# Optimization experiments

Measured on AMD Instinct MI355X. Metric: run time of the kernel, lower is better.

## Reference

```python
import jax, jax.numpy as jnp
import numpy as np

B, N, M, D, NHEAD, FF, C, K = 2, 16384, 2048, 256, 8, 512, 50, 3
HID = 128          # embed/pos hidden
HEAD_HID = 256     # seg head hidden
L = 4              # depth
EPS = 1e-5


def setup_inputs() -> dict:
    key = jax.random.key(0)
    ks = jax.random.split(key, 32)
    g = lambda i, shape: jax.random.normal(ks[i], shape, dtype=jnp.float32) * 0.02
    z = lambda shape: jnp.zeros(shape, jnp.float32)
    o = lambda shape: jnp.ones(shape, jnp.float32)
    return {
        "xyz": jax.random.normal(ks[0], (B, N, 3), dtype=jnp.float32),
        "embed_w1": g(1, (3, HID)), "embed_b1": z((HID,)),
        "embed_w2": g(2, (HID, D)), "embed_b2": z((D,)),
        "pos_w1": g(3, (3, HID)), "pos_b1": z((HID,)),
        "pos_w2": g(4, (HID, D)), "pos_b2": z((D,)),
        "Wq": g(5, (L, D, D)), "bq": z((L, D)),
        "Wk": g(6, (L, D, D)), "bk": z((L, D)),
        "Wv": g(7, (L, D, D)), "bv": z((L, D)),
        "Wo": g(8, (L, D, D)), "bo": z((L, D)),
        "ln1_s": o((L, D)), "ln1_b": z((L, D)),
        "W1": g(9, (L, D, FF)), "b1": z((L, FF)),
        "W2": g(10, (L, FF, D)), "b2": z((L, D)),
        "ln2_s": o((L, D)), "ln2_b": z((L, D)),
        "head_w1": g(11, (D, HEAD_HID)), "head_b1": z((HEAD_HID,)),
        "head_w2": g(12, (HEAD_HID, C)), "head_b2": z((C,)),
    }


def _ln(x, s, b):
    m = x.mean(-1, keepdims=True)
    v = ((x - m) ** 2).mean(-1, keepdims=True)
    return (x - m) / jnp.sqrt(v + EPS) * s + b


def reference(xyz, embed_w1, embed_b1, embed_w2, embed_b2,
              pos_w1, pos_b1, pos_w2, pos_b2,
              Wq, bq, Wk, bk, Wv, bv, Wo, bo, ln1_s, ln1_b,
              W1, b1, W2, b2, ln2_s, ln2_b,
              head_w1, head_b1, head_w2, head_b2):
    # deterministic token subsample (replaces randperm stub): strided pick of M points
    stride = N // M
    tok = xyz[:, ::stride, :][:, :M]                                  # [B,M,3]
    # per-point embed + learned positional encoding
    x = jax.nn.relu(tok @ embed_w1 + embed_b1) @ embed_w2 + embed_b2  # [B,M,D]
    x = x + jax.nn.relu(tok @ pos_w1 + pos_b1) @ pos_w2 + pos_b2
    dh = D // NHEAD
    scale = 1.0 / jnp.sqrt(jnp.float32(dh))

    def layer(x, p):
        wq, bq_, wk, bk_, wv, bv_, wo, bo_, l1s, l1b, w1, b1_, w2, b2_, l2s, l2b = p
        # pre-norm MHSA
        y = _ln(x, l1s, l1b)
        q = (y @ wq + bq_).reshape(B, M, NHEAD, dh)
        k = (y @ wk + bk_).reshape(B, M, NHEAD, dh)
        v = (y @ wv + bv_).reshape(B, M, NHEAD, dh)
        att = jax.nn.softmax(jnp.einsum('bqhd,bkhd->bhqk', q, k) * scale, axis=-1)
        o = jnp.einsum('bhqk,bkhd->bqhd', att, v).reshape(B, M, D)
        x = x + o @ wo + bo_
        # pre-norm FFN (gelu, exact erf as in torch)
        y = _ln(x, l2s, l2b)
        x = x + jax.nn.gelu(y @ w1 + b1_, approximate=False) @ w2 + b2_
        return x, None

    x, _ = jax.lax.scan(layer, x, (Wq, bq, Wk, bk, Wv, bv, Wo, bo,
                                   ln1_s, ln1_b, W1, b1, W2, b2, ln2_s, ln2_b))
    logits_tok = jax.nn.relu(x @ head_w1 + head_b1) @ head_w2 + head_b2  # [B,M,C]

    # kNN propagation N->M: dist^2 = |q|^2 + |k|^2 - 2 q.k, topk smallest
    q2 = (xyz ** 2).sum(-1)[..., None]            # [B,N,1]
    k2 = (tok ** 2).sum(-1)[:, None, :]           # [B,1,M]
    dist = q2 + k2 - 2.0 * jnp.einsum('bnd,bmd->bnm', xyz, tok)
    dist = jax.lax.stop_gradient(jnp.maximum(dist, 0.0))
    idx = jax.lax.top_k(-dist, K)[1]              # [B,N,K]
    logits_nk = logits_tok[jnp.arange(B)[:, None, None], idx]  # [B,N,K,C]
    return logits_nk.mean(axis=2)                 # [B,N,C]
```

## Files before the change

kernel.cpp:

```cpp
#include <hip/hip_runtime.h>
#include <hip/hip_bf16.h>
#include <math.h>

#define B_ 2
#define N_ 16384
#define M_ 2048
#define D_ 256
#define NHEAD_ 8
#define DH_ 32
#define FF_ 512
#define C_ 50
#define HID_ 128
#define HHID_ 256
#define L_ 4
#define EPS_ 1e-5f
#define TOK_ (B_*M_)
#define QSCALE_ 0.25507604155757994f

typedef short short8 __attribute__((ext_vector_type(8)));
typedef short short4_t __attribute__((ext_vector_type(4)));
typedef float f32x4 __attribute__((ext_vector_type(4)));

__device__ __forceinline__ short f2bf(float f) {
  union { float f; unsigned u; } c; c.f = f;
  unsigned u = c.u;
  unsigned r = (u + 0x7FFFu + ((u >> 16) & 1u)) >> 16;
  return (short)r;
}
__device__ __forceinline__ float fast_exp2(float x) {
  float r;
  asm("v_exp_f32 %0, %1" : "=v"(r) : "v"(x));
  return r;
}
__device__ __forceinline__ unsigned cvt_pk_bf16(float lo, float hi) {
  unsigned r;
  asm("v_cvt_pk_bf16_f32 %0, %1, %2" : "=v"(r) : "v"(lo), "v"(hi));
  return r;
}

__device__ __forceinline__ void stage16(const short* __restrict__ g, short* lds,
                                        int rowStride, int tid) {
  int row = tid >> 2, gr = tid & 3;
  int kg = gr ^ (row & 3);
  __builtin_amdgcn_global_load_lds(
      (const __attribute__((address_space(1))) void*)(g + (size_t)row * rowStride + kg * 8),
      (__attribute__((address_space(3))) void*)(lds + tid * 8),
      16, 0, 0);
}

__global__ __launch_bounds__(256) void wconv_all(
    const float* __restrict__ Wq, const float* __restrict__ Wk,
    const float* __restrict__ Wv, const float* __restrict__ Wo,
    const float* __restrict__ W1, const float* __restrict__ W2,
    const float* __restrict__ h1,
    short* __restrict__ WqT, short* __restrict__ WkT,
    short* __restrict__ WvT, short* __restrict__ WoT,
    short* __restrict__ W1T, short* __restrict__ W2T, short* __restrict__ h1T) {
  int bid = blockIdx.x;
  const float* W; short* WT; int Kd, Nd, tn, tk;
  if (bid < 256) {
    int mat = bid >> 6, rem = bid & 63, l = rem >> 4, t = rem & 15;
    W  = (mat == 0 ? Wq : mat == 1 ? Wk : mat == 2 ? Wv : Wo) + l * 65536;
    WT = (mat == 0 ? WqT : mat == 1 ? WkT : mat == 2 ? WvT : WoT) + l * 65536;
    Kd = 256; Nd = 256; tn = t & 3; tk = t >> 2;
  } else if (bid < 384) {
    int rem = bid - 256, l = rem >> 5, t = rem & 31;
    W = W1 + l * 131072; WT = W1T + l * 131072;
    Kd = 256; Nd = 512; tn = t & 7; tk = t >> 3;
  } else if (bid < 512) {
    int rem = bid - 384, l = rem >> 5, t = rem & 31;
    W = W2 + l * 131072; WT = W2T + l * 131072;
    Kd = 512; Nd = 256; tn = t & 3; tk = t >> 2;
  } else {
    int t = bid - 512;
    W = h1; WT = h1T; Kd = 256; Nd = 256; tn = t & 3; tk = t >> 2;
  }
  int n0 = tn * 64, k0 = tk * 64;
  __shared__ short ts[64][72];
  int tid = threadIdx.x;
  #pragma unroll
  for (int i = 0; i < 4; ++i) {
    int r = i * 16 + (tid >> 4);
    int c4 = (tid & 15) * 4;
    float4 v = *(const float4*)&W[(size_t)(k0 + r) * Nd + n0 + c4];
    ts[c4 + 0][r] = f2bf(v.x);
    ts[c4 + 1][r] = f2bf(v.y);
    ts[c4 + 2][r] = f2bf(v.z);
    ts[c4 + 3][r] = f2bf(v.w);
  }
  __syncthreads();
  #pragma unroll
  for (int i = 0; i < 2; ++i) {
    int n = i * 32 + (tid >> 3);
    int kc = (tid & 7) * 8;
    *(short8*)&WT[(size_t)(n0 + n) * Kd + k0 + kc] = *(short8*)&ts[n][kc];
  }
}

__global__ __launch_bounds__(128) void embed_kernel(
    const float* __restrict__ xyz,
    const float* __restrict__ ew1, const float* __restrict__ eb1,
    const float* __restrict__ ew2, const float* __restrict__ eb2,
    const float* __restrict__ pw1, const float* __restrict__ pb1,
    const float* __restrict__ pw2, const float* __restrict__ pb2,
    float* __restrict__ x) {
  int t = blockIdx.x;
  int b = t / M_, m = t % M_;
  const float* p = xyz + ((size_t)b * N_ + (size_t)m * 8) * 3;
  float t0 = p[0], t1 = p[1], t2 = p[2];
  __shared__ float he[HID_], hp[HID_];
  int j = threadIdx.x;
  {
    float a = fmaf(t0, ew1[j], fmaf(t1, ew1[HID_ + j], fmaf(t2, ew1[2 * HID_ + j], eb1[j])));
    he[j] = fmaxf(a, 0.f);
    float c = fmaf(t0, pw1[j], fmaf(t1, pw1[HID_ + j], fmaf(t2, pw1[2 * HID_ + j], pb1[j])));
    hp[j] = fmaxf(c, 0.f);
  }
  __syncthreads();
  for (int d = j; d < D_; d += HID_) {
    float acc = eb2[d] + pb2[d];
    for (int k = 0; k < HID_; ++k) {
      acc = fmaf(he[k], ew2[k * D_ + d], acc);
      acc = fmaf(hp[k], pw2[k * D_ + d], acc);
    }
    x[(size_t)t * D_ + d] = acc;
  }
}

__global__ __launch_bounds__(256) void ln_fused(
    const float* __restrict__ x, const float* __restrict__ pa,
    const float* __restrict__ pb, const float* __restrict__ bias,
    const float* __restrict__ s, const float* __restrict__ bb,
    float* __restrict__ xw, short* __restrict__ y16) {
  int r = blockIdx.x * 4 + (threadIdx.x >> 6);
  int t = threadIdx.x & 63;
  float4 v = ((const float4*)(x + (size_t)r * D_))[t];
  if (pa) {
    float4 a = ((const float4*)(pa + (size_t)r * D_))[t];
    float4 c = ((const float4*)(pb + (size_t)r * D_))[t];
    float4 bi = ((const float4*)bias)[t];
    v.x += a.x + c.x + bi.x;
    v.y += a.y + c.y + bi.y;
    v.z += a.z + c.z + bi.z;
    v.w += a.w + c.w + bi.w;
    ((float4*)(xw + (size_t)r * D_))[t] = v;
  }
  float sum = v.x + v.y + v.z + v.w;
  #pragma unroll
  for (int o = 1; o < 64; o <<= 1) sum += __shfl_xor(sum, o, 64);
  float mean = sum * (1.f / D_);
  float dx = v.x - mean, dy = v.y - mean, dz = v.z - mean, dw = v.w - mean;
  float vs = dx * dx + dy * dy + dz * dz + dw * dw;
  #pragma unroll
  for (int o = 1; o < 64; o <<= 1) vs += __shfl_xor(vs, o, 64);
  float inv = 1.0f / sqrtf(vs * (1.f / D_) + EPS_);
  float4 sv = ((const float4*)s)[t];
  float4 bv = ((const float4*)bb)[t];
  short4_t ov;
  ov[0] = f2bf(dx * inv * sv.x + bv.x);
  ov[1] = f2bf(dy * inv * sv.y + bv.y);
  ov[2] = f2bf(dz * inv * sv.z + bv.z);
  ov[3] = f2bf(dw * inv * sv.w + bv.w);
  *(short4_t*)(y16 + (size_t)r * D_ + t * 4) = ov;
}

__global__ __launch_bounds__(256) void head2_kernel(
    const float* __restrict__ pa, const float* __restrict__ pb,
    const float* __restrict__ b1h, const float* __restrict__ w2,
    const float* __restrict__ b2, float* __restrict__ lt) {
  __shared__ float ys[4][HHID_];
  int w = threadIdx.x >> 6, l = threadIdx.x & 63;
  int t = blockIdx.x * 4 + w;
  float4 a = ((const float4*)(pa + (size_t)t * HHID_))[l];
  float4 c = ((const float4*)(pb + (size_t)t * HHID_))[l];
  float4 bi = ((const float4*)b1h)[l];
  float4 v;
  v.x = fmaxf(a.x + c.x + bi.x, 0.f);
  v.y = fmaxf(a.y + c.y + bi.y, 0.f);
  v.z = fmaxf(a.z + c.z + bi.z, 0.f);
  v.w = fmaxf(a.w + c.w + bi.w, 0.f);
  *(float4*)&ys[w][l * 4] = v;
  int cc = l < C_ ? l : 0;
  float a0 = 0.f, a1 = 0.f, a2 = 0.f, a3 = 0.f;
  #pragma unroll 4
  for (int k = 0; k < HHID_; k += 4) {
    a0 = fmaf(ys[w][k + 0], w2[(k + 0) * C_ + cc], a0);
    a1 = fmaf(ys[w][k + 1], w2[(k + 1) * C_ + cc], a1);
    a2 = fmaf(ys[w][k + 2], w2[(k + 2) * C_ + cc], a2);
    a3 = fmaf(ys[w][k + 3], w2[(k + 3) * C_ + cc], a3);
  }
  if (l < C_) lt[(size_t)t * C_ + l] = (a0 + a1) + (a2 + a3) + b2[l];
}

template <int ACT, int RES>
__device__ __forceinline__ void gemm16_body(
    const short* __restrict__ A16, const short* __restrict__ WT,
    const float* __restrict__ bias, const float* __restrict__ R,
    float* __restrict__ C, short* __restrict__ C16, short* __restrict__ VT,
    float oscale, int K, int Ncols, int m0, int n0) {
  __shared__ short As[64][32];
  __shared__ short Bs[64][32];
  int tid = threadIdx.x;
  int w = tid >> 6, l = tid & 63;
  int lq = l & 15, lg = l >> 4;
  int wr = (w & 1) * 32, wc = (w >> 1) * 32;
  int ga = (lg ^ (lq & 3)) * 8;
  f32x4 acc00 = {0.f, 0.f, 0.f, 0.f};
  f32x4 acc01 = {0.f, 0.f, 0.f, 0.f};
  f32x4 acc10 = {0.f, 0.f, 0.f, 0.f};
  f32x4 acc11 = {0.f, 0.f, 0.f, 0.f};
  for (int kk = 0; kk < K; kk += 32) {
    __syncthreads();
    stage16(A16 + (size_t)m0 * K + kk, &As[0][0], K, tid);
    stage16(WT + (size_t)n0 * K + kk, &Bs[0][0], K, tid);
    __syncthreads();
    short8 a0 = *(short8*)&As[wr + lq][ga];
    short8 a1 = *(short8*)&As[wr + 16 + lq][ga];
    short8 b0 = *(short8*)&Bs[wc + lq][ga];
    short8 b1 = *(short8*)&Bs[wc + 16 + lq][ga];
    acc00 = __builtin_amdgcn_mfma_f32_16x16x32_bf16(a0, b0, acc00, 0, 0, 0);
    acc01 = __builtin_amdgcn_mfma_f32_16x16x32_bf16(a0, b1, acc01, 0, 0, 0);
    acc10 = __builtin_amdgcn_mfma_f32_16x16x32_bf16(a1, b0, acc10, 0, 0, 0);
    acc11 = __builtin_amdgcn_mfma_f32_16x16x32_bf16(a1, b1, acc11, 0, 0, 0);
  }
  #pragma unroll
  for (int fi = 0; fi < 2; ++fi) {
    int row = m0 + wr + fi * 16 + lg * 4;
    #pragma unroll
    for (int fj = 0; fj < 2; ++fj) {
      int col = n0 + wc + fj * 16 + lq;
      short4_t vt4;
      #pragma unroll
      for (int r = 0; r < 4; ++r) {
        float v = (fi == 0 ? (fj == 0 ? acc00[r] : acc01[r])
                           : (fj == 0 ? acc10[r] : acc11[r])) + bias[col];
        if (ACT == 1) v = fmaxf(v, 0.f);
        else if (ACT == 2) v = 0.5f * v * (1.f + erff(v * 0.70710678118654752f));
        if (RES) v += R[(size_t)(row + r) * Ncols + col];
        if (C)   C[(size_t)(row + r) * Ncols + col] = v;
        if (C16) C16[(size_t)(row + r) * Ncols + col] = f2bf(v * oscale);
        if (VT)  vt4[r] = f2bf(v);
      }
      if (VT) {
        int bb = row >> 11, mm = row & (M_ - 1);
        *(short4_t*)&VT[((size_t)(bb * 256 + col)) * M_ + mm] = vt4;
      }
    }
  }
}

template <int ACT, int RES>
__global__ __launch_bounds__(256) void gemm16(
    const short* __restrict__ A16, const short* __restrict__ WT,
    const float* __restrict__ bias, const float* __restrict__ R,
    float* __restrict__ C, short* __restrict__ C16,
    int K, int Ncols) {
  gemm16_body<ACT, RES>(A16, WT, bias, R, C, C16, nullptr, 1.f, K, Ncols,
                        blockIdx.y * 64, blockIdx.x * 64);
}

__global__ __launch_bounds__(256) void gemm16_part(
    const short* __restrict__ A16, const short* __restrict__ WT,
    float* __restrict__ P, int K, int Klen, int Ncols) {
  __shared__ short As[64][32];
  __shared__ short Bs[64][32];
  int tid = threadIdx.x;
  int w = tid >> 6, l = tid & 63;
  int lq = l & 15, lg = l >> 4;
  int wr = (w & 1) * 32, wc = (w >> 1) * 32;
  int ga = (lg ^ (lq & 3)) * 8;
  int m0 = blockIdx.y * 64, n0 = blockIdx.x * 64;
  int k0 = blockIdx.z * Klen;
  f32x4 acc00 = {0.f, 0.f, 0.f, 0.f};
  f32x4 acc01 = {0.f, 0.f, 0.f, 0.f};
  f32x4 acc10 = {0.f, 0.f, 0.f, 0.f};
  f32x4 acc11 = {0.f, 0.f, 0.f, 0.f};
  for (int kk = k0; kk < k0 + Klen; kk += 32) {
    __syncthreads();
    stage16(A16 + (size_t)m0 * K + kk, &As[0][0], K, tid);
    stage16(WT + (size_t)n0 * K + kk, &Bs[0][0], K, tid);
    __syncthreads();
    short8 a0 = *(short8*)&As[wr + lq][ga];
    short8 a1 = *(short8*)&As[wr + 16 + lq][ga];
    short8 b0 = *(short8*)&Bs[wc + lq][ga];
    short8 b1 = *(short8*)&Bs[wc + 16 + lq][ga];
    acc00 = __builtin_amdgcn_mfma_f32_16x16x32_bf16(a0, b0, acc00, 0, 0, 0);
    acc01 = __builtin_amdgcn_mfma_f32_16x16x32_bf16(a0, b1, acc01, 0, 0, 0);
    acc10 = __builtin_amdgcn_mfma_f32_16x16x32_bf16(a1, b0, acc10, 0, 0, 0);
    acc11 = __builtin_amdgcn_mfma_f32_16x16x32_bf16(a1, b1, acc11, 0, 0, 0);
  }
  float* Pp = P + (size_t)blockIdx.z * TOK_ * Ncols;
  #pragma unroll
  for (int fi = 0; fi < 2; ++fi) {
    int row = m0 + wr + fi * 16 + lg * 4;
    #pragma unroll
    for (int fj = 0; fj < 2; ++fj) {
      int col = n0 + wc + fj * 16 + lq;
      #pragma unroll
      for (int r = 0; r < 4; ++r) {
        float v = (fi == 0 ? (fj == 0 ? acc00[r] : acc01[r])
                           : (fj == 0 ? acc10[r] : acc11[r]));
        Pp[(size_t)(row + r) * Ncols + col] = v;
      }
    }
  }
}

__global__ __launch_bounds__(256) void qkv16(
    const short* __restrict__ A16,
    const short* __restrict__ WqT, const short* __restrict__ WkT, const short* __restrict__ WvT,
    const float* __restrict__ bq, const float* __restrict__ bk, const float* __restrict__ bv,
    short* __restrict__ q16, short* __restrict__ k16, short* __restrict__ vt16) {
  int sel = blockIdx.x >> 2;
  int n0 = (blockIdx.x & 3) << 6;
  int m0 = blockIdx.y * 64;
  if (sel == 0) {
    gemm16_body<0, 0>(A16, WqT, bq, nullptr, nullptr, q16, nullptr, QSCALE_, D_, D_, m0, n0);
  } else if (sel == 1) {
    gemm16_body<0, 0>(A16, WkT, bk, nullptr, nullptr, k16, nullptr, 1.f, D_, D_, m0, n0);
  } else {
    gemm16_body<0, 0>(A16, WvT, bv, nullptr, nullptr, nullptr, vt16, 1.f, D_, D_, m0, n0);
  }
}

__global__ __launch_bounds__(256) void wo_split(
    const float* __restrict__ po0, const float* __restrict__ po1,
    const float* __restrict__ po2, const float* __restrict__ po3,
    const float* __restrict__ pl, const short* __restrict__ WT,
    float* __restrict__ P) {
  __shared__ short As[64][136];
  __shared__ short Bs[64][32];
  int tid = threadIdx.x;
  int w = tid >> 6, l = tid & 63;
  int m0 = blockIdx.y * 64, n0 = blockIdx.x * 64;
  int half = blockIdx.z;
  int c2 = l * 2;
  int hh = half * 4 + (c2 >> 5);
  int d0 = c2 & 31;
  #pragma unroll 4
  for (int c = 0; c < 16; ++c) {
    int t = w * 16 + c;
    int row = m0 + t;
    int bb = row >> 11, mm = row & (M_ - 1);
    size_t f = (size_t)(bb * NHEAD_ + hh) * M_ + mm;
    float inv = 1.f / (pl[f] + pl[16 * M_ + f] + pl[32 * M_ + f] + pl[48 * M_ + f]);
    float v0 = (po0[f * 32 + d0] + po1[f * 32 + d0] + po2[f * 32 + d0] + po3[f * 32 + d0]) * inv;
    float v1 = (po0[f * 32 + d0 + 1] + po1[f * 32 + d0 + 1] + po2[f * 32 + d0 + 1] + po3[f * 32 + d0 + 1]) * inv;
    *(unsigned*)&As[t][c2] = cvt_pk_bf16(v0, v1);
  }
  int lq = l & 15, lg = l >> 4;
  int wr = (w & 1) * 32, wc = (w >> 1) * 32;
  int gb = (lg ^ (lq & 3)) * 8;
  f32x4 acc00 = {0.f, 0.f, 0.f, 0.f};
  f32x4 acc01 = {0.f, 0.f, 0.f, 0.f};
  f32x4 acc10 = {0.f, 0.f, 0.f, 0.f};
  f32x4 acc11 = {0.f, 0.f, 0.f, 0.f};
  for (int kk = 0; kk < 128; kk += 32) {
    __syncthreads();
    stage16(WT + (size_t)n0 * D_ + half * 128 + kk, &Bs[0][0], D_, tid);
    __syncthreads();
    short8 a0 = *(short8*)&As[wr + lq][kk + lg * 8];
    short8 a1 = *(short8*)&As[wr + 16 + lq][kk + lg * 8];
    short8 b0 = *(short8*)&Bs[wc + lq][gb];
    short8 b1 = *(short8*)&Bs[wc + 16 + lq][gb];
    acc00 = __builtin_amdgcn_mfma_f32_16x16x32_bf16(a0, b0, acc00, 0, 0, 0);
    acc01 = __builtin_amdgcn_mfma_f32_16x16x32_bf16(a0, b1, acc01, 0, 0, 0);
    acc10 = __builtin_amdgcn_mfma_f32_16x16x32_bf16(a1, b0, acc10, 0, 0, 0);
    acc11 = __builtin_amdgcn_mfma_f32_16x16x32_bf16(a1, b1, acc11, 0, 0, 0);
  }
  float* Pp = P + (size_t)half * TOK_ * D_;
  #pragma unroll
  for (int fi = 0; fi < 2; ++fi) {
    int row = m0 + wr + fi * 16 + lg * 4;
    #pragma unroll
    for (int fj = 0; fj < 2; ++fj) {
      int col = n0 + wc + fj * 16 + lq;
      #pragma unroll
      for (int r = 0; r < 4; ++r) {
        float v = (fi == 0 ? (fj == 0 ? acc00[r] : acc01[r])
                           : (fj == 0 ? acc10[r] : acc11[r]));
        Pp[(size_t)(row + r) * D_ + col] = v;
      }
    }
  }
}

#define KSTR 40
#define VSTR 72
#define PSTR 72
__global__ __launch_bounds__(256) void attn_mfma_kernel(
    const short* __restrict__ q16, const short* __restrict__ k16,
    const short* __restrict__ vt16,
    float* __restrict__ po0, float* __restrict__ po1,
    float* __restrict__ po2, float* __restrict__ po3,
    float* __restrict__ pl) {
  __shared__ short Ks[64][KSTR];
  __shared__ short Vt[32][VSTR];
  __shared__ short Ps[4][16][PSTR];
  int bid = blockIdx.x;
  int quar = bid & 3;
  int qt = (bid >> 2) & 31;
  int h  = (bid >> 7) & 7;
  int b  = bid >> 10;
  int tid = threadIdx.x;
  int w  = tid >> 6;
  int l  = tid & 63;
  int lq = l & 15;
  int lg = l >> 4;

  short8 qf = *(const short8*)&q16[(size_t)(b * M_ + qt * 64 + w * 16 + lq) * D_ + h * DH_ + lg * 8];

  float l_i = 0.f;
  f32x4 o0 = {0.f, 0.f, 0.f, 0.f};
  f32x4 o1 = {0.f, 0.f, 0.f, 0.f};
  int srow = tid >> 2, scol = (tid & 3) * 8;
  int vd = tid >> 3, vm = (tid & 7) * 8;
  const short* kp = k16 + (size_t)(b * M_ + quar * 512 + srow) * D_ + h * DH_ + scol;
  const short* vp = vt16 + (size_t)((b * NHEAD_ + h) * DH_ + vd) * M_ + quar * 512 + vm;

  for (int kt = 0; kt < 8; ++kt) {
    __syncthreads();
    *(short8*)&Ks[srow][scol] = *(const short8*)(kp + (size_t)(kt * 64) * D_);
    *(short8*)&Vt[vd][vm]     = *(const short8*)(vp + kt * 64);
    __syncthreads();
    f32x4 st[4];
    #pragma unroll
    for (int t = 0; t < 4; ++t) {
      short8 kf = *(short8*)&Ks[t * 16 + lq][lg * 8];
      f32x4 z = {0.f, 0.f, 0.f, 0.f};
      st[t] = __builtin_amdgcn_mfma_f32_16x16x32_bf16(kf, qf, z, 0, 0, 0);
    }
    #pragma unroll
    for (int t = 0; t < 4; ++t)
      #pragma unroll
      for (int r2 = 0; r2 < 4; ++r2) {
        st[t][r2] = fast_exp2(st[t][r2]);
        l_i += st[t][r2];
      }
    {
      unsigned* pw = (unsigned*)&Ps[w][lq][0];
      #pragma unroll
      for (int t = 0; t < 4; ++t) {
        uint2 pk;
        pk.x = cvt_pk_bf16(st[t][0], st[t][1]);
        pk.y = cvt_pk_bf16(st[t][2], st[t][3]);
        *(uint2*)(pw + t * 8 + lg * 2) = pk;
      }
    }
    #pragma unroll
    for (int c = 0; c < 2; ++c) {
      short8 pf = *(short8*)&Ps[w][lq][c * 32 + lg * 8];
      short8 v0 = *(short8*)&Vt[lq][c * 32 + lg * 8];
      short8 v1 = *(short8*)&Vt[16 + lq][c * 32 + lg * 8];
      o0 = __builtin_amdgcn_mfma_f32_16x16x32_bf16(v0, pf, o0, 0, 0, 0);
      o1 = __builtin_amdgcn_mfma_f32_16x16x32_bf16(v1, pf, o1, 0, 0, 0);
    }
  }
  l_i += __shfl_xor(l_i, 16, 64);
  l_i += __shfl_xor(l_i, 32, 64);
  int f = (b * NHEAD_ + h) * M_ + qt * 64 + w * 16 + lq;
  float* pp = (quar == 0 ? po0 : quar == 1 ? po1 : quar == 2 ? po2 : po3) + (size_t)f * 32;
  #pragma unroll
  for (int r2 = 0; r2 < 4; ++r2) pp[lg * 4 + r2] = o0[r2];
  #pragma unroll
  for (int r2 = 0; r2 < 4; ++r2) pp[16 + lg * 4 + r2] = o1[r2];
  if (lg == 0) pl[quar * (16 * M_) + f] = l_i;
}

__global__ __launch_bounds__(512) void knn_kernel(
    const float* __restrict__ xyz, const float* __restrict__ lt,
    float* __restrict__ out) {
  __shared__ float4 tok[2064];
  int b = blockIdx.x >> 9;
  int q0 = (blockIdx.x & 511) << 5;
  int tid = threadIdx.x;
  for (int i = tid; i < M_; i += 512) {
    const float* tp = xyz + ((size_t)b * N_ + (size_t)i * 8) * 3;
    float a = tp[0], bb = tp[1], cc = tp[2];
    tok[i + (i >> 7)] = make_float4(a, bb, cc, a * a + bb * bb + cc * cc);
  }
  __syncthreads();
  int g = tid >> 4, sl = tid & 15;
  int n = q0 + g;
  const float* qp = xyz + ((size_t)b * N_ + n) * 3;
  float qx = qp[0], qy = qp[1], qz = qp[2];
  float q2 = qx * qx + qy * qy + qz * qz;
  float dd0 = INFINITY, dd1 = INFINITY, dd2 = INFINITY;
  int ii0 = 0, ii1 = 0, ii2 = 0;
  const float4* cp = &tok[sl * 129];
  int mb = sl << 7;
  #pragma unroll 2
  for (int j = 0; j < 128; ++j) {
    float4 t = cp[j];
    float dot = fmaf(qx, t.x, fmaf(qy, t.y, qz * t.z));
    float d = fmaxf(q2 + t.w - 2.f * dot, 0.f);
    if (d < dd2) {
      int m = mb + j;
      if (d < dd1) {
        dd2 = dd1; ii2 = ii1;
        if (d < dd0) { dd1 = dd0; ii1 = ii0; dd0 = d; ii0 = m; }
        else         { dd1 = d;  ii1 = m; }
      } else         { dd2 = d;  ii2 = m; }
    }
  }
  auto insT = [&](float d, int i) {
    if (d < dd2 || (d == dd2 && i < ii2)) {
      if (d < dd1 || (d == dd1 && i < ii1)) {
        dd2 = dd1; ii2 = ii1;
        if (d < dd0 || (d == dd0 && i < ii0)) { dd1 = dd0; ii1 = ii0; dd0 = d; ii0 = i; }
        else { dd1 = d; ii1 = i; }
      } else { dd2 = d; ii2 = i; }
    }
  };
  #pragma unroll
  for (int off = 1; off < 16; off <<= 1) {
    float p0 = __shfl_xor(dd0, off, 64); int pi0 = __shfl_xor(ii0, off, 64);
    float p1 = __shfl_xor(dd1, off, 64); int pi1 = __shfl_xor(ii1, off, 64);
    float p2 = __shfl_xor(dd2, off, 64); int pi2 = __shfl_xor(ii2, off, 64);
    insT(p0, pi0); insT(p1, pi1); insT(p2, pi2);
  }
  const float* l0 = lt + ((size_t)b * M_ + ii0) * C_;
  const float* l1 = lt + ((size_t)b * M_ + ii1) * C_;
  const float* l2 = lt + ((size_t)b * M_ + ii2) * C_;
  float* op = out + ((size_t)b * N_ + n) * C_;
  for (int cc = sl; cc < C_; cc += 16)
    op[cc] = (l0[cc] + l1[cc] + l2[cc]) * (1.f / 3.f);
}

extern "C" void kernel_launch(void* const* d_in, const int* in_sizes, int n_in,
                              void* d_out, int out_size, void* d_ws, size_t ws_size,
                              hipStream_t stream) {
  const float* xyz  = (const float*)d_in[0];
  const float* ew1  = (const float*)d_in[1];
  const float* eb1  = (const float*)d_in[2];
  const float* ew2  = (const float*)d_in[3];
  const float* eb2  = (const float*)d_in[4];
  const float* pw1  = (const float*)d_in[5];
  const float* pb1  = (const float*)d_in[6];
  const float* pw2  = (const float*)d_in[7];
  const float* pb2  = (const float*)d_in[8];
  const float* Wq   = (const float*)d_in[9];
  const float* bq   = (const float*)d_in[10];
  const float* Wk   = (const float*)d_in[11];
  const float* bk   = (const float*)d_in[12];
  const float* Wv   = (const float*)d_in[13];
  const float* bv   = (const float*)d_in[14];
  const float* Wo   = (const float*)d_in[15];
  const float* bo   = (const float*)d_in[16];
  const float* ln1s = (const float*)d_in[17];
  const float* ln1b = (const float*)d_in[18];
  const float* W1   = (const float*)d_in[19];
  const float* b1   = (const float*)d_in[20];
  const float* W2   = (const float*)d_in[21];
  const float* b2   = (const float*)d_in[22];
  const float* ln2s = (const float*)d_in[23];
  const float* ln2b = (const float*)d_in[24];
  const float* hw1  = (const float*)d_in[25];
  const float* hb1  = (const float*)d_in[26];
  const float* hw2  = (const float*)d_in[27];
  const float* hb2  = (const float*)d_in[28];
  float* out = (float*)d_out;

  float* x   = (float*)d_ws;
  float* y   = x + 1048576;
  float* po2 = y + 1048576;
  float* po3 = po2 + 1048576;
  float* lt  = po3 + 1048576;
  short* y16 = (short*)(lt + 204800);
  short* q16 = y16 + 1048576;
  short* k16 = q16 + 1048576;
  short* v16 = k16 + 1048576;
  short* vt16 = v16 + 1048576;
  short* ob16 = vt16 + 1048576;
  short* x16  = ob16 + 1048576;
  short* ff16 = x16 + 1048576;
  short* WqT = ff16 + 2097152;
  short* WkT = WqT + 262144;
  short* WvT = WkT + 262144;
  short* WoT = WvT + 262144;
  short* W1T = WoT + 262144;
  short* W2T = W1T + 524288;
  short* h1T = W2T + 524288;
  float* wpart = (float*)(h1T + 65536);
  float* po0 = y;
  float* po1 = (float*)ff16;
  float* pl  = lt;

  wconv_all<<<528, 256, 0, stream>>>(Wq, Wk, Wv, Wo, W1, W2, hw1,
                                     WqT, WkT, WvT, WoT, W1T, W2T, h1T);
  embed_kernel<<<TOK_, 128, 0, stream>>>(xyz, ew1, eb1, ew2, eb2, pw1, pb1, pw2, pb2, x);

  dim3 gQKV(12, TOK_ / 64);
  dim3 gDs(D_ / 64, TOK_ / 64, 2);
  dim3 gF(FF_ / 64, TOK_ / 64);
  dim3 gD(D_ / 64, TOK_ / 64);
  for (int l = 0; l < L_; ++l) {
    if (l == 0)
      ln_fused<<<TOK_ / 4, 256, 0, stream>>>(x, nullptr, nullptr, nullptr,
                                             ln1s + l * D_, ln1b + l * D_, x, y16);
    else
      ln_fused<<<TOK_ / 4, 256, 0, stream>>>(x, wpart, wpart + (size_t)TOK_ * D_,
                                             b2 + (l - 1) * D_,
                                             ln1s + l * D_, ln1b + l * D_, x, y16);
    qkv16<<<gQKV, 256, 0, stream>>>(y16, WqT + l * 65536, WkT + l * 65536, WvT + l * 65536,
                                    bq + l * D_, bk + l * D_, bv + l * D_, q16, k16, vt16);
    attn_mfma_kernel<<<2048, 256, 0, stream>>>(q16, k16, vt16, po0, po1, po2, po3, pl);
    wo_split<<<gDs, 256, 0, stream>>>(po0, po1, po2, po3, pl, WoT + l * 65536, wpart);
    ln_fused<<<TOK_ / 4, 256, 0, stream>>>(x, wpart, wpart + (size_t)TOK_ * D_,
                                           bo + l * D_,
                                           ln2s + l * D_, ln2b + l * D_, x, y16);
    gemm16<2, 0><<<gF, 256, 0, stream>>>(y16, W1T + l * 131072, b1 + l * FF_, nullptr, nullptr, ff16, D_, FF_);
    if (l < L_ - 1) {
      gemm16_part<<<gDs, 256, 0, stream>>>(ff16, W2T + l * 131072, wpart, FF_, 256, D_);
    } else {
      gemm16<0, 1><<<gD, 256, 0, stream>>>(ff16, W2T + l * 131072, b2 + l * D_, x, x, x16, FF_, D_);
    }
  }
  gemm16_part<<<gDs, 256, 0, stream>>>(x16, h1T, wpart, D_, 128, HHID_);
  head2_kernel<<<TOK_ / 4, 256, 0, stream>>>(wpart, wpart + (size_t)TOK_ * HHID_,
                                             hb1, hw2, hb2, lt);
  knn_kernel<<<1024, 512, 0, stream>>>(xyz, lt, out);
}
```

Before: 384.1 us.

## Split attention keys into two halves with 128-key tiles instead of four quarters

The attention kernel now splits the key range into two halves of 1024 keys instead of four quarters of 512, and processes 128 keys per iteration rather than 64, launching half as many blocks. This halves the partial-output and partial-sum traffic written by attention and read back by the Wo projection. It also halves the barrier count per key. In exchange there are fewer blocks for parallelism (1024), a larger LDS footprint per block, and more live score registers per thread.

```diff
diff --git a/kernel.cpp b/kernel.cpp
--- a/kernel.cpp
+++ b/kernel.cpp
@@ -325,7 +325,6 @@
 
 __global__ __launch_bounds__(256) void wo_split(
     const float* __restrict__ po0, const float* __restrict__ po1,
-    const float* __restrict__ po2, const float* __restrict__ po3,
     const float* __restrict__ pl, const short* __restrict__ WT,
     float* __restrict__ P) {
   __shared__ short As[64][136];
@@ -343,9 +342,9 @@
     int row = m0 + t;
     int bb = row >> 11, mm = row & (M_ - 1);
     size_t f = (size_t)(bb * NHEAD_ + hh) * M_ + mm;
-    float inv = 1.f / (pl[f] + pl[16 * M_ + f] + pl[32 * M_ + f] + pl[48 * M_ + f]);
-    float v0 = (po0[f * 32 + d0] + po1[f * 32 + d0] + po2[f * 32 + d0] + po3[f * 32 + d0]) * inv;
-    float v1 = (po0[f * 32 + d0 + 1] + po1[f * 32 + d0 + 1] + po2[f * 32 + d0 + 1] + po3[f * 32 + d0 + 1]) * inv;
+    float inv = 1.f / (pl[f] + pl[16 * M_ + f]);
+    float v0 = (po0[f * 32 + d0] + po1[f * 32 + d0]) * inv;
+    float v1 = (po0[f * 32 + d0 + 1] + po1[f * 32 + d0 + 1]) * inv;
     *(unsigned*)&As[t][c2] = cvt_pk_bf16(v0, v1);
   }
   int lq = l & 15, lg = l >> 4;
@@ -385,23 +384,19 @@
   }
 }
 
-#define KSTR 40
-#define VSTR 72
-#define PSTR 72
 __global__ __launch_bounds__(256) void attn_mfma_kernel(
     const short* __restrict__ q16, const short* __restrict__ k16,
     const short* __restrict__ vt16,
     float* __restrict__ po0, float* __restrict__ po1,
-    float* __restrict__ po2, float* __restrict__ po3,
     float* __restrict__ pl) {
-  __shared__ short Ks[64][KSTR];
-  __shared__ short Vt[32][VSTR];
-  __shared__ short Ps[4][16][PSTR];
+  __shared__ short Ks[128][40];
+  __shared__ short Vt[32][136];
+  __shared__ short Ps[4][16][136];
   int bid = blockIdx.x;
-  int quar = bid & 3;
-  int qt = (bid >> 2) & 31;
-  int h  = (bid >> 7) & 7;
-  int b  = bid >> 10;
+  int half = bid & 1;
+  int qt = (bid >> 1) & 31;
+  int h  = (bid >> 6) & 7;
+  int b  = bid >> 9;
   int tid = threadIdx.x;
   int w  = tid >> 6;
   int l  = tid & 63;
@@ -413,25 +408,31 @@
   float l_i = 0.f;
   f32x4 o0 = {0.f, 0.f, 0.f, 0.f};
   f32x4 o1 = {0.f, 0.f, 0.f, 0.f};
-  int srow = tid >> 2, scol = (tid & 3) * 8;
-  int vd = tid >> 3, vm = (tid & 7) * 8;
-  const short* kp = k16 + (size_t)(b * M_ + quar * 512 + srow) * D_ + h * DH_ + scol;
-  const short* vp = vt16 + (size_t)((b * NHEAD_ + h) * DH_ + vd) * M_ + quar * 512 + vm;
+  int srow = tid >> 1, scol = (tid & 1) * 16;
+  int vd = tid >> 3, vm = (tid & 7) * 16;
+  const short* kp = k16 + (size_t)(b * M_ + half * 1024 + srow) * D_ + h * DH_ + scol;
+  const short* vp = vt16 + (size_t)((b * NHEAD_ + h) * DH_ + vd) * M_ + half * 1024 + vm;
 
   for (int kt = 0; kt < 8; ++kt) {
     __syncthreads();
-    *(short8*)&Ks[srow][scol] = *(const short8*)(kp + (size_t)(kt * 64) * D_);
-    *(short8*)&Vt[vd][vm]     = *(const short8*)(vp + kt * 64);
-    __syncthreads();
-    f32x4 st[4];
+    {
+      const short* kg = kp + (size_t)(kt * 128) * D_;
+      *(short8*)&Ks[srow][scol]     = *(const short8*)(kg);
+      *(short8*)&Ks[srow][scol + 8] = *(const short8*)(kg + 8);
+      const short* vg = vp + kt * 128;
+      *(short8*)&Vt[vd][vm]     = *(const short8*)(vg);
+      *(short8*)&Vt[vd][vm + 8] = *(const short8*)(vg + 8);
+    }
+    __syncthreads();
+    f32x4 st[8];
     #pragma unroll
-    for (int t = 0; t < 4; ++t) {
+    for (int t = 0; t < 8; ++t) {
       short8 kf = *(short8*)&Ks[t * 16 + lq][lg * 8];
       f32x4 z = {0.f, 0.f, 0.f, 0.f};
       st[t] = __builtin_amdgcn_mfma_f32_16x16x32_bf16(kf, qf, z, 0, 0, 0);
     }
     #pragma unroll
-    for (int t = 0; t < 4; ++t)
+    for (int t = 0; t < 8; ++t)
       #pragma unroll
       for (int r2 = 0; r2 < 4; ++r2) {
         st[t][r2] = fast_exp2(st[t][r2]);
@@ -440,7 +441,7 @@
     {
       unsigned* pw = (unsigned*)&Ps[w][lq][0];
       #pragma unroll
-      for (int t = 0; t < 4; ++t) {
+      for (int t = 0; t < 8; ++t) {
         uint2 pk;
         pk.x = cvt_pk_bf16(st[t][0], st[t][1]);
         pk.y = cvt_pk_bf16(st[t][2], st[t][3]);
@@ -448,7 +449,7 @@
       }
     }
     #pragma unroll
-    for (int c = 0; c < 2; ++c) {
+    for (int c = 0; c < 4; ++c) {
       short8 pf = *(short8*)&Ps[w][lq][c * 32 + lg * 8];
       short8 v0 = *(short8*)&Vt[lq][c * 32 + lg * 8];
       short8 v1 = *(short8*)&Vt[16 + lq][c * 32 + lg * 8];
@@ -459,12 +460,12 @@
   l_i += __shfl_xor(l_i, 16, 64);
   l_i += __shfl_xor(l_i, 32, 64);
   int f = (b * NHEAD_ + h) * M_ + qt * 64 + w * 16 + lq;
-  float* pp = (quar == 0 ? po0 : quar == 1 ? po1 : quar == 2 ? po2 : po3) + (size_t)f * 32;
+  float* pp = (half == 0 ? po0 : po1) + (size_t)f * 32;
   #pragma unroll
   for (int r2 = 0; r2 < 4; ++r2) pp[lg * 4 + r2] = o0[r2];
   #pragma unroll
   for (int r2 = 0; r2 < 4; ++r2) pp[16 + lg * 4 + r2] = o1[r2];
-  if (lg == 0) pl[quar * (16 * M_) + f] = l_i;
+  if (lg == 0) pl[half * (16 * M_) + f] = l_i;
 }
 
 __global__ __launch_bounds__(512) void knn_kernel(
@@ -604,8 +605,8 @@
                                              ln1s + l * D_, ln1b + l * D_, x, y16);
     qkv16<<<gQKV, 256, 0, stream>>>(y16, WqT + l * 65536, WkT + l * 65536, WvT + l * 65536,
                                     bq + l * D_, bk + l * D_, bv + l * D_, q16, k16, vt16);
-    attn_mfma_kernel<<<2048, 256, 0, stream>>>(q16, k16, vt16, po0, po1, po2, po3, pl);
-    wo_split<<<gDs, 256, 0, stream>>>(po0, po1, po2, po3, pl, WoT + l * 65536, wpart);
+    attn_mfma_kernel<<<1024, 256, 0, stream>>>(q16, k16, vt16, po0, po1, pl);
+    wo_split<<<gDs, 256, 0, stream>>>(po0, po1, pl, WoT + l * 65536, wpart);
     ln_fused<<<TOK_ / 4, 256, 0, stream>>>(x, wpart, wpart + (size_t)TOK_ * D_,
                                            bo + l * D_,
                                            ln2s + l * D_, ln2b + l * D_, x, y16);
```

Result: no change. 378.3 us (-1.5%).
